# Kernel tuning notes

Measured on AMD Instinct MI355X. Metric: run time of the kernel, lower is better.

The kernel has to match this reference:

```python
import jax, jax.numpy as jnp
import numpy as np

# Production-scale dims
B, DZ, NW, NH, K = 8, 32, 48, 48, 25          # batch, dim_z, grid width/height, n_objects_max
W_RAW = H_RAW = 384.0                          # raw image size
SIZE_MIN, SIZE_MAX = 12.0, 48.0                # object size bounds
SCORE_T, OVER_T = 0.1, 0.3                     # score_threshold, overlap_threshold


def _conv1x1(x, w, b):
    # x: (B, d, nW, nH), w: (o, d), b: (o,) -> (B, o, nW, nH)  [Decoder1by1Linear]
    return jnp.einsum('bdwh,od->bowh', x, w) + b[None, :, None, None]


def _to_box_list(x):
    # (B, nW, nH) -> (N, B) with N = nW*nH, matching convert_to_box_list's permute(2,3,0,1).view
    return jnp.transpose(x, (1, 2, 0)).reshape(-1, x.shape[0])


def _nms(probT, x1, y1, x2, y2, k_max, score_t, over_t):
    # probT, x1..y2: (B, N). Greedy score/overlap NMS -> idx (B, K) int32, mask (B, N) float
    area = (x2 - x1) * (y2 - y1)
    xi1 = jnp.maximum(x1[:, :, None], x1[:, None, :])
    yi1 = jnp.maximum(y1[:, :, None], y1[:, None, :])
    xi2 = jnp.minimum(x2[:, :, None], x2[:, None, :])
    yi2 = jnp.minimum(y2[:, :, None], y2[:, None, :])
    inter = jnp.clip(xi2 - xi1, 0.0) * jnp.clip(yi2 - yi1, 0.0)
    union = area[:, :, None] + area[:, None, :] - inter
    iou = inter / jnp.maximum(union, 1e-8)                      # (B, N, N)
    possible0 = probT > score_t
    Bsz, N = probT.shape
    idx0 = jnp.zeros((Bsz, k_max), jnp.int32)
    val0 = jnp.zeros((Bsz, k_max), bool)

    def body(k, carry):
        possible, idxb, valb = carry
        masked = jnp.where(possible, probT, -jnp.inf)
        sel = jnp.argmax(masked, axis=1).astype(jnp.int32)      # (B,)
        ok = jnp.take_along_axis(possible, sel[:, None], axis=1)[:, 0]
        row = jnp.take_along_axis(iou, sel[:, None, None], axis=1)[:, 0, :]
        possible = possible & (row <= over_t)                   # suppresses sel itself (IoU=1)
        return possible, idxb.at[:, k].set(sel), valb.at[:, k].set(ok)

    _, idxb, valb = jax.lax.fori_loop(0, k_max, body, (possible0, idx0, val0))
    mask = jnp.zeros((Bsz, N), probT.dtype).at[jnp.arange(Bsz)[:, None], idxb].max(
        valb.astype(probT.dtype))
    return idxb, mask


def setup_inputs() -> dict:
    key = jax.random.key(0)
    ks = jax.random.split(key, 5)
    return {
        'zwhere_sample': jax.random.normal(ks[0], (B, DZ, NW, NH), jnp.float32),
        'w_zwhere': 0.2 * jax.random.normal(ks[1], (4, DZ), jnp.float32),
        'b_zwhere': jnp.zeros((4,), jnp.float32),
        'logit_sample': jax.random.normal(ks[2], (B, DZ, NW, NH), jnp.float32),
        'w_logit': 0.2 * jax.random.normal(ks[3], (1, DZ), jnp.float32),
        'b_logit': jnp.zeros((1,), jnp.float32),
        'weight_logits': jax.random.normal(ks[4], (K, B, 1, int(W_RAW), int(H_RAW)), jnp.float32),
    }


def reference(zwhere_sample, w_zwhere, b_zwhere, logit_sample, w_logit, b_logit, weight_logits):
    nW, nH = zwhere_sample.shape[-2:]
    # --- box decoding from zwhere latent map ---
    t = jax.nn.sigmoid(_conv1x1(zwhere_sample, w_zwhere, b_zwhere))  # (B,4,nW,nH)
    tx, ty, tw, th = t[:, 0], t[:, 1], t[:, 2], t[:, 3]
    ix = jnp.arange(nW, dtype=t.dtype)[:, None]   # ij meshgrid rows
    iy = jnp.arange(nH, dtype=t.dtype)[None, :]
    bx = W_RAW * (ix + tx) / nW
    by = H_RAW * (iy + ty) / nH
    bw = SIZE_MIN + (SIZE_MAX - SIZE_MIN) * tw
    bh = SIZE_MIN + (SIZE_MAX - SIZE_MIN) * th
    bx_l, by_l = _to_box_list(bx), _to_box_list(by)   # (N, B)
    bw_l, bh_l = _to_box_list(bw), _to_box_list(bh)
    # --- probability map from logit latent map ---
    p_map = jax.nn.sigmoid(_conv1x1(logit_sample, w_logit, b_logit))  # (B,1,nW,nH)
    prob_all = _to_box_list(p_map[:, 0])              # (N, B)
    probT = prob_all.T                                 # (B, N)
    x1 = (bx_l - 0.5 * bw_l).T
    x2 = (bx_l + 0.5 * bw_l).T
    y1 = (by_l - 0.5 * bh_l).T
    y2 = (by_l + 0.5 * bh_l).T
    # --- NMS under stop_gradient (torch.no_grad in original) ---
    sg = jax.lax.stop_gradient
    idxb, maskB = _nms(sg(probT), sg(x1), sg(y1), sg(x2), sg(y2), K, SCORE_T, OVER_T)
    # prob_few = gather(prob_all * nms_mask, index_top_k): differentiable w.r.t. prob_all
    prob_few = jnp.take_along_axis(probT * maskB, idxb, axis=1).T   # (K, B)
    # --- mask compositing (from_weights_to_masks over the object dim) ---
    big_weight = jax.nn.softplus(weight_logits)       # (K, B, 1, W, H)
    sum_w = jnp.sum(big_weight, axis=0, keepdims=True)
    big_mask = jnp.tanh(sum_w) * (big_weight / jnp.clip(sum_w, 1e-6))
    # probability-weighted masks (downstream compositing)
    return prob_few[:, :, None, None, None] * big_mask  # (K, B, 1, W, H)
```

## Files before the change

kernel.cpp:

```cpp
#include <hip/hip_runtime.h>
#include <math.h>

#define BATCH 8
#define DZ    32
#define NWH   48
#define NBOX  (NWH*NWH)
#define KMAX  25
#define PIX   (384*384)
#define NTOT  (BATCH*NBOX)
#define SLOTS (NBOX/256)

__device__ __forceinline__ float sigm(float x) { return 1.0f / (1.0f + expf(-x)); }

__device__ __forceinline__ float sp_fast(float x) {
    return fmaxf(x, 0.0f) + __logf(1.0f + __expf(-fabsf(x)));
}

__global__ __launch_bounds__(256) void box_kernel(
    const float* __restrict__ z, const float* __restrict__ wz, const float* __restrict__ bz,
    const float* __restrict__ lg, const float* __restrict__ wl, const float* __restrict__ bl,
    float* __restrict__ ws)
{
    int t = blockIdx.x * 256 + threadIdx.x;
    int b = t / 576, j = t % 576;
    int iw = j / 12, ihq = j % 12;

    const float* zb = z  + (((size_t)b * DZ) * NWH + iw) * NWH + ihq * 4;
    const float* lb = lg + (((size_t)b * DZ) * NWH + iw) * NWH + ihq * 4;

    float b0 = bz[0], b1 = bz[1], b2 = bz[2], b3 = bz[3], blg = bl[0];
    float4 a0 = make_float4(b0,b0,b0,b0);
    float4 a1 = make_float4(b1,b1,b1,b1);
    float4 a2 = make_float4(b2,b2,b2,b2);
    float4 a3 = make_float4(b3,b3,b3,b3);
    float4 al = make_float4(blg,blg,blg,blg);

    #pragma unroll 8
    for (int d = 0; d < DZ; ++d) {
        float4 zv = *(const float4*)(zb + (size_t)d * NBOX);
        float4 lv = *(const float4*)(lb + (size_t)d * NBOX);
        float w0 = wz[d], w1 = wz[32+d], w2 = wz[64+d], w3 = wz[96+d], wv = wl[d];
        a0.x += zv.x*w0; a0.y += zv.y*w0; a0.z += zv.z*w0; a0.w += zv.w*w0;
        a1.x += zv.x*w1; a1.y += zv.y*w1; a1.z += zv.z*w1; a1.w += zv.w*w1;
        a2.x += zv.x*w2; a2.y += zv.y*w2; a2.z += zv.z*w2; a2.w += zv.w*w2;
        a3.x += zv.x*w3; a3.y += zv.y*w3; a3.z += zv.z*w3; a3.w += zv.w*w3;
        al.x += lv.x*wv; al.y += lv.y*wv; al.z += lv.z*wv; al.w += lv.w*wv;
    }

    float4 X1, Y1, X2, Y2, P;
    float txv[4] = {a0.x,a0.y,a0.z,a0.w};
    float tyv[4] = {a1.x,a1.y,a1.z,a1.w};
    float twv[4] = {a2.x,a2.y,a2.z,a2.w};
    float thv[4] = {a3.x,a3.y,a3.z,a3.w};
    float alv[4] = {al.x,al.y,al.z,al.w};
    float x1o[4], y1o[4], x2o[4], y2o[4], po[4];
    #pragma unroll
    for (int c = 0; c < 4; ++c) {
        float tx = sigm(txv[c]), ty = sigm(tyv[c]), tw = sigm(twv[c]), th = sigm(thv[c]);
        float bx = 8.0f * ((float)iw + tx);
        float by = 8.0f * ((float)(ihq*4 + c) + ty);
        float bw = 12.0f + 36.0f * tw;
        float bh = 12.0f + 36.0f * th;
        x1o[c] = bx - 0.5f*bw;  y1o[c] = by - 0.5f*bh;
        x2o[c] = bx + 0.5f*bw;  y2o[c] = by + 0.5f*bh;
        po[c]  = sigm(alv[c]);
    }
    X1 = make_float4(x1o[0],x1o[1],x1o[2],x1o[3]);
    Y1 = make_float4(y1o[0],y1o[1],y1o[2],y1o[3]);
    X2 = make_float4(x2o[0],x2o[1],x2o[2],x2o[3]);
    Y2 = make_float4(y2o[0],y2o[1],y2o[2],y2o[3]);
    P  = make_float4(po[0], po[1], po[2], po[3]);

    int o = b * NBOX + iw * NWH + ihq * 4;
    *(float4*)(ws + 0*NTOT + o) = X1;
    *(float4*)(ws + 1*NTOT + o) = Y1;
    *(float4*)(ws + 2*NTOT + o) = X2;
    *(float4*)(ws + 3*NTOT + o) = Y2;
    *(float4*)(ws + 4*NTOT + o) = P;
}

__global__ __launch_bounds__(256) void nms_kernel(const float* __restrict__ ws,
                                                  float* __restrict__ pf)
{
    __shared__ float4 boxS[NBOX];
    __shared__ float  prS[NBOX];
    __shared__ float  redv[4];
    __shared__ int    redi[4];
    __shared__ float4 selB;
    __shared__ int    idxA[KMAX];
    __shared__ int    okA[KMAX];

    int b = blockIdx.x, tid = threadIdx.x;

    float x1r[SLOTS], y1r[SLOTS], x2r[SLOTS], y2r[SLOTS], arr[SLOTS], mkv[SLOTS];
    #pragma unroll
    for (int s = 0; s < SLOTS; ++s) {
        int n = tid + 256*s;
        int o = b * NBOX + n;
        float x1 = ws[0*NTOT+o], y1 = ws[1*NTOT+o], x2 = ws[2*NTOT+o], y2 = ws[3*NTOT+o];
        float p  = ws[4*NTOT+o];
        x1r[s]=x1; y1r[s]=y1; x2r[s]=x2; y2r[s]=y2;
        arr[s] = (x2-x1)*(y2-y1);
        mkv[s] = (p > 0.1f) ? p : -INFINITY;
        boxS[n] = make_float4(x1,y1,x2,y2);
        prS[n]  = p;
    }
    __syncthreads();

    for (int k = 0; k < KMAX; ++k) {
        float4 sb = make_float4(0,0,0,0); float sar = 0.f;
        if (k > 0) { sb = selB; sar = (sb.z - sb.x) * (sb.w - sb.y); }

        float bv = -INFINITY; int bi = 0;
        #pragma unroll
        for (int s = 0; s < SLOTS; ++s) {
            if (k > 0 && mkv[s] != -INFINITY) {
                float xi1 = fmaxf(sb.x, x1r[s]);
                float yi1 = fmaxf(sb.y, y1r[s]);
                float xi2 = fminf(sb.z, x2r[s]);
                float yi2 = fminf(sb.w, y2r[s]);
                float inter = fmaxf(xi2 - xi1, 0.f) * fmaxf(yi2 - yi1, 0.f);
                float uni   = sar + arr[s] - inter;
                float iou   = inter / fmaxf(uni, 1e-8f);
                if (iou > 0.3f) mkv[s] = -INFINITY;
            }
            float v = mkv[s];
            if (v > bv) { bv = v; bi = tid + 256*s; }
        }
        #pragma unroll
        for (int off = 32; off > 0; off >>= 1) {
            float ov = __shfl_down(bv, off);
            int   oi = __shfl_down(bi, off);
            if (ov > bv || (ov == bv && oi < bi)) { bv = ov; bi = oi; }
        }
        if ((tid & 63) == 0) { redv[tid >> 6] = bv; redi[tid >> 6] = bi; }
        __syncthreads();
        if (tid == 0) {
            for (int w = 1; w < 4; ++w)
                if (redv[w] > bv || (redv[w] == bv && redi[w] < bi)) { bv = redv[w]; bi = redi[w]; }
            idxA[k] = bi;
            okA[k]  = (bv != -INFINITY) ? 1 : 0;
            selB    = boxS[bi];
        }
        __syncthreads();
    }

    if (tid == 0) {
        #pragma unroll 1
        for (int k = 0; k < KMAX; ++k) {
            float m = 0.f;
            for (int k2 = 0; k2 < KMAX; ++k2)
                if (idxA[k2] == idxA[k] && okA[k2]) m = 1.f;
            pf[k * BATCH + b] = prS[idxA[k]] * m;
        }
    }
}

__global__ __launch_bounds__(256) void big_kernel(const float* __restrict__ wlg,
                                                  const float* __restrict__ pf,
                                                  float* __restrict__ out)
{
    const size_t stride = (size_t)BATCH * PIX;
    size_t j = ((size_t)blockIdx.x * 256 + threadIdx.x) * 4;
    int b = (int)(j / PIX);

    float4 sp[KMAX];
    float sx = 0.f, sy = 0.f, sz = 0.f, sw = 0.f;
    #pragma unroll
    for (int k = 0; k < KMAX; ++k) {
        float4 v = *(const float4*)(wlg + (size_t)k * stride + j);
        float4 t;
        t.x = sp_fast(v.x); t.y = sp_fast(v.y); t.z = sp_fast(v.z); t.w = sp_fast(v.w);
        sp[k] = t;
        sx += t.x; sy += t.y; sz += t.z; sw += t.w;
    }
    float4 m;
    {
        float tx = __expf(-2.f*sx), ty = __expf(-2.f*sy), tz = __expf(-2.f*sz), tw = __expf(-2.f*sw);
        m.x = (1.f - tx) * __builtin_amdgcn_rcpf(1.f + tx) * __builtin_amdgcn_rcpf(fmaxf(sx, 1e-6f));
        m.y = (1.f - ty) * __builtin_amdgcn_rcpf(1.f + ty) * __builtin_amdgcn_rcpf(fmaxf(sy, 1e-6f));
        m.z = (1.f - tz) * __builtin_amdgcn_rcpf(1.f + tz) * __builtin_amdgcn_rcpf(fmaxf(sz, 1e-6f));
        m.w = (1.f - tw) * __builtin_amdgcn_rcpf(1.f + tw) * __builtin_amdgcn_rcpf(fmaxf(sw, 1e-6f));
    }
    #pragma unroll
    for (int k = 0; k < KMAX; ++k) {
        float c = pf[k * BATCH + b];
        float4 o;
        o.x = c * m.x * sp[k].x;
        o.y = c * m.y * sp[k].y;
        o.z = c * m.z * sp[k].z;
        o.w = c * m.w * sp[k].w;
        *(float4*)(out + (size_t)k * stride + j) = o;
    }
}

extern "C" void kernel_launch(void* const* d_in, const int* in_sizes, int n_in,
                              void* d_out, int out_size, void* d_ws, size_t ws_size,
                              hipStream_t stream)
{
    const float* zwhere = (const float*)d_in[0];
    const float* w_zw   = (const float*)d_in[1];
    const float* b_zw   = (const float*)d_in[2];
    const float* logit  = (const float*)d_in[3];
    const float* w_lg   = (const float*)d_in[4];
    const float* b_lg   = (const float*)d_in[5];
    const float* wlogit = (const float*)d_in[6];
    float* out = (float*)d_out;
    float* ws  = (float*)d_ws;
    float* pf  = ws + 5 * NTOT;

    box_kernel<<<(BATCH*576)/256, 256, 0, stream>>>(zwhere, w_zw, b_zw, logit, w_lg, b_lg, ws);
    nms_kernel<<<BATCH, 256, 0, stream>>>(ws, pf);
    const int n4 = BATCH * PIX / 4;
    big_kernel<<<n4 / 256, 256, 0, stream>>>(wlogit, pf, out);
}
```

Measured before the change: 108.9 us.

## Fuse box and NMS kernels, pack argmax keys, half-precision softplus cache

Measured after the change: 234.9 us. 116% more time.

```diff
diff --git a/kernel.cpp b/kernel.cpp
--- a/kernel.cpp
+++ b/kernel.cpp
@@ -1,4 +1,5 @@
 #include <hip/hip_runtime.h>
+#include <hip/hip_fp16.h>
 #include <math.h>
 
 #define BATCH 8
@@ -7,190 +8,154 @@
 #define NBOX  (NWH*NWH)
 #define KMAX  25
 #define PIX   (384*384)
-#define NTOT  (BATCH*NBOX)
-#define SLOTS (NBOX/256)
+#define NTHR  576
+#define NW9   9
+
+typedef float vfloat4 __attribute__((ext_vector_type(4)));
 
 __device__ __forceinline__ float sigm(float x) { return 1.0f / (1.0f + expf(-x)); }
-
 __device__ __forceinline__ float sp_fast(float x) {
     return fmaxf(x, 0.0f) + __logf(1.0f + __expf(-fabsf(x)));
 }
 
-__global__ __launch_bounds__(256) void box_kernel(
+__global__ __launch_bounds__(NTHR) void boxnms_kernel(
     const float* __restrict__ z, const float* __restrict__ wz, const float* __restrict__ bz,
     const float* __restrict__ lg, const float* __restrict__ wl, const float* __restrict__ bl,
-    float* __restrict__ ws)
+    float* __restrict__ pfT)
 {
-    int t = blockIdx.x * 256 + threadIdx.x;
-    int b = t / 576, j = t % 576;
-    int iw = j / 12, ihq = j % 12;
+    __shared__ vfloat4 boxS[NBOX];
+    __shared__ float   prS[NBOX];
+    __shared__ unsigned long long keyB[2][NW9];
+    __shared__ int idxA[KMAX], okA[KMAX];
+
+    const int b = blockIdx.x, t = threadIdx.x;
+    const int iw = t / 12, ihq = t % 12;
 
     const float* zb = z  + (((size_t)b * DZ) * NWH + iw) * NWH + ihq * 4;
     const float* lb = lg + (((size_t)b * DZ) * NWH + iw) * NWH + ihq * 4;
-
     float b0 = bz[0], b1 = bz[1], b2 = bz[2], b3 = bz[3], blg = bl[0];
-    float4 a0 = make_float4(b0,b0,b0,b0);
-    float4 a1 = make_float4(b1,b1,b1,b1);
-    float4 a2 = make_float4(b2,b2,b2,b2);
-    float4 a3 = make_float4(b3,b3,b3,b3);
-    float4 al = make_float4(blg,blg,blg,blg);
-
+    vfloat4 a0 = {b0,b0,b0,b0}, a1 = {b1,b1,b1,b1}, a2 = {b2,b2,b2,b2},
+            a3 = {b3,b3,b3,b3}, al = {blg,blg,blg,blg};
     #pragma unroll 8
     for (int d = 0; d < DZ; ++d) {
-        float4 zv = *(const float4*)(zb + (size_t)d * NBOX);
-        float4 lv = *(const float4*)(lb + (size_t)d * NBOX);
+        vfloat4 zv = *(const vfloat4*)(zb + (size_t)d * NBOX);
+        vfloat4 lv = *(const vfloat4*)(lb + (size_t)d * NBOX);
         float w0 = wz[d], w1 = wz[32+d], w2 = wz[64+d], w3 = wz[96+d], wv = wl[d];
-        a0.x += zv.x*w0; a0.y += zv.y*w0; a0.z += zv.z*w0; a0.w += zv.w*w0;
-        a1.x += zv.x*w1; a1.y += zv.y*w1; a1.z += zv.z*w1; a1.w += zv.w*w1;
-        a2.x += zv.x*w2; a2.y += zv.y*w2; a2.z += zv.z*w2; a2.w += zv.w*w2;
-        a3.x += zv.x*w3; a3.y += zv.y*w3; a3.z += zv.z*w3; a3.w += zv.w*w3;
-        al.x += lv.x*wv; al.y += lv.y*wv; al.z += lv.z*wv; al.w += lv.w*wv;
+        a0 += zv * w0; a1 += zv * w1; a2 += zv * w2; a3 += zv * w3; al += lv * wv;
     }
 
-    float4 X1, Y1, X2, Y2, P;
-    float txv[4] = {a0.x,a0.y,a0.z,a0.w};
-    float tyv[4] = {a1.x,a1.y,a1.z,a1.w};
-    float twv[4] = {a2.x,a2.y,a2.z,a2.w};
-    float thv[4] = {a3.x,a3.y,a3.z,a3.w};
-    float alv[4] = {al.x,al.y,al.z,al.w};
-    float x1o[4], y1o[4], x2o[4], y2o[4], po[4];
-    #pragma unroll
-    for (int c = 0; c < 4; ++c) {
-        float tx = sigm(txv[c]), ty = sigm(tyv[c]), tw = sigm(twv[c]), th = sigm(thv[c]);
-        float bx = 8.0f * ((float)iw + tx);
-        float by = 8.0f * ((float)(ihq*4 + c) + ty);
-        float bw = 12.0f + 36.0f * tw;
-        float bh = 12.0f + 36.0f * th;
-        x1o[c] = bx - 0.5f*bw;  y1o[c] = by - 0.5f*bh;
-        x2o[c] = bx + 0.5f*bw;  y2o[c] = by + 0.5f*bh;
-        po[c]  = sigm(alv[c]);
+    float x1r[4], y1r[4], x2r[4], y2r[4], arr[4], mkv[4];
+    int   nbs[4];
+    {
+        float t0v[4] = {a0.x,a0.y,a0.z,a0.w};
+        float t1v[4] = {a1.x,a1.y,a1.z,a1.w};
+        float t2v[4] = {a2.x,a2.y,a2.z,a2.w};
+        float t3v[4] = {a3.x,a3.y,a3.z,a3.w};
+        float alv[4] = {al.x,al.y,al.z,al.w};
+        #pragma unroll
+        for (int c = 0; c < 4; ++c) {
+            float tx = sigm(t0v[c]), ty = sigm(t1v[c]), tw = sigm(t2v[c]), th = sigm(t3v[c]);
+            float bx = 8.0f * ((float)iw + tx);
+            float by = 8.0f * ((float)(ihq*4 + c) + ty);
+            float bw = 12.0f + 36.0f * tw;
+            float bh = 12.0f + 36.0f * th;
+            float x1 = bx - 0.5f*bw, y1 = by - 0.5f*bh, x2 = bx + 0.5f*bw, y2 = by + 0.5f*bh;
+            float p  = sigm(alv[c]);
+            int   n  = iw * NWH + ihq*4 + c;
+            x1r[c]=x1; y1r[c]=y1; x2r[c]=x2; y2r[c]=y2;
+            arr[c] = (x2-x1)*(y2-y1);
+            mkv[c] = (p > 0.1f) ? p : -INFINITY;
+            nbs[c] = n;
+            boxS[n] = (vfloat4){x1,y1,x2,y2};
+            prS[n]  = p;
+        }
     }
-    X1 = make_float4(x1o[0],x1o[1],x1o[2],x1o[3]);
-    Y1 = make_float4(y1o[0],y1o[1],y1o[2],y1o[3]);
-    X2 = make_float4(x2o[0],x2o[1],x2o[2],x2o[3]);
-    Y2 = make_float4(y2o[0],y2o[1],y2o[2],y2o[3]);
-    P  = make_float4(po[0], po[1], po[2], po[3]);
 
-    int o = b * NBOX + iw * NWH + ihq * 4;
-    *(float4*)(ws + 0*NTOT + o) = X1;
-    *(float4*)(ws + 1*NTOT + o) = Y1;
-    *(float4*)(ws + 2*NTOT + o) = X2;
-    *(float4*)(ws + 3*NTOT + o) = Y2;
-    *(float4*)(ws + 4*NTOT + o) = P;
-}
-
-__global__ __launch_bounds__(256) void nms_kernel(const float* __restrict__ ws,
-                                                  float* __restrict__ pf)
-{
-    __shared__ float4 boxS[NBOX];
-    __shared__ float  prS[NBOX];
-    __shared__ float  redv[4];
-    __shared__ int    redi[4];
-    __shared__ float4 selB;
-    __shared__ int    idxA[KMAX];
-    __shared__ int    okA[KMAX];
-
-    int b = blockIdx.x, tid = threadIdx.x;
-
-    float x1r[SLOTS], y1r[SLOTS], x2r[SLOTS], y2r[SLOTS], arr[SLOTS], mkv[SLOTS];
-    #pragma unroll
-    for (int s = 0; s < SLOTS; ++s) {
-        int n = tid + 256*s;
-        int o = b * NBOX + n;
-        float x1 = ws[0*NTOT+o], y1 = ws[1*NTOT+o], x2 = ws[2*NTOT+o], y2 = ws[3*NTOT+o];
-        float p  = ws[4*NTOT+o];
-        x1r[s]=x1; y1r[s]=y1; x2r[s]=x2; y2r[s]=y2;
-        arr[s] = (x2-x1)*(y2-y1);
-        mkv[s] = (p > 0.1f) ? p : -INFINITY;
-        boxS[n] = make_float4(x1,y1,x2,y2);
-        prS[n]  = p;
-    }
-    __syncthreads();
-
+    float sx1=0.f, sy1=0.f, sx2=0.f, sy2=0.f, sar=0.f;
     for (int k = 0; k < KMAX; ++k) {
-        float4 sb = make_float4(0,0,0,0); float sar = 0.f;
-        if (k > 0) { sb = selB; sar = (sb.z - sb.x) * (sb.w - sb.y); }
-
-        float bv = -INFINITY; int bi = 0;
+        unsigned long long best = 0ULL;
         #pragma unroll
-        for (int s = 0; s < SLOTS; ++s) {
-            if (k > 0 && mkv[s] != -INFINITY) {
-                float xi1 = fmaxf(sb.x, x1r[s]);
-                float yi1 = fmaxf(sb.y, y1r[s]);
-                float xi2 = fminf(sb.z, x2r[s]);
-                float yi2 = fminf(sb.w, y2r[s]);
+        for (int c = 0; c < 4; ++c) {
+            if (k > 0 && mkv[c] != -INFINITY) {
+                float xi1 = fmaxf(sx1, x1r[c]);
+                float yi1 = fmaxf(sy1, y1r[c]);
+                float xi2 = fminf(sx2, x2r[c]);
+                float yi2 = fminf(sy2, y2r[c]);
                 float inter = fmaxf(xi2 - xi1, 0.f) * fmaxf(yi2 - yi1, 0.f);
-                float uni   = sar + arr[s] - inter;
+                float uni   = sar + arr[c] - inter;
                 float iou   = inter / fmaxf(uni, 1e-8f);
-                if (iou > 0.3f) mkv[s] = -INFINITY;
+                if (iou > 0.3f) mkv[c] = -INFINITY;
             }
-            float v = mkv[s];
-            if (v > bv) { bv = v; bi = tid + 256*s; }
+            if (mkv[c] != -INFINITY) {
+                unsigned long long kk =
+                    ((unsigned long long)__float_as_uint(mkv[c]) << 32) | (unsigned int)(~nbs[c]);
+                if (kk > best) best = kk;
+            }
         }
         #pragma unroll
         for (int off = 32; off > 0; off >>= 1) {
-            float ov = __shfl_down(bv, off);
-            int   oi = __shfl_down(bi, off);
-            if (ov > bv || (ov == bv && oi < bi)) { bv = ov; bi = oi; }
+            unsigned long long o = __shfl_down(best, off);
+            if (o > best) best = o;
         }
-        if ((tid & 63) == 0) { redv[tid >> 6] = bv; redi[tid >> 6] = bi; }
+        if ((t & 63) == 0) keyB[k & 1][t >> 6] = best;
         __syncthreads();
-        if (tid == 0) {
-            for (int w = 1; w < 4; ++w)
-                if (redv[w] > bv || (redv[w] == bv && redi[w] < bi)) { bv = redv[w]; bi = redi[w]; }
-            idxA[k] = bi;
-            okA[k]  = (bv != -INFINITY) ? 1 : 0;
-            selB    = boxS[bi];
+        unsigned long long m = keyB[k & 1][0];
+        #pragma unroll
+        for (int w = 1; w < NW9; ++w) {
+            unsigned long long o = keyB[k & 1][w];
+            if (o > m) m = o;
         }
-        __syncthreads();
+        int sel = (m == 0ULL) ? 0 : (int)(~(unsigned int)(m & 0xFFFFFFFFULL));
+        if (t == 0) { idxA[k] = sel; okA[k] = (m != 0ULL); }
+        vfloat4 sb = boxS[sel];
+        sx1 = sb.x; sy1 = sb.y; sx2 = sb.z; sy2 = sb.w;
+        sar = (sx2 - sx1) * (sy2 - sy1);
     }
 
-    if (tid == 0) {
+    if (t == 0) {
         #pragma unroll 1
         for (int k = 0; k < KMAX; ++k) {
-            float m = 0.f;
+            float mm = 0.f;
             for (int k2 = 0; k2 < KMAX; ++k2)
-                if (idxA[k2] == idxA[k] && okA[k2]) m = 1.f;
-            pf[k * BATCH + b] = prS[idxA[k]] * m;
+                if (idxA[k2] == idxA[k] && okA[k2]) mm = 1.f;
+            pfT[b * 32 + k] = prS[idxA[k]] * mm;
         }
     }
 }
 
-__global__ __launch_bounds__(256) void big_kernel(const float* __restrict__ wlg,
-                                                  const float* __restrict__ pf,
-                                                  float* __restrict__ out)
+__global__ __launch_bounds__(256, 6) void big_kernel(const float* __restrict__ wlg,
+                                                     const float* __restrict__ pfT,
+                                                     float* __restrict__ out)
 {
     const size_t stride = (size_t)BATCH * PIX;
     size_t j = ((size_t)blockIdx.x * 256 + threadIdx.x) * 4;
     int b = (int)(j / PIX);
 
-    float4 sp[KMAX];
+    __half2 sp01[KMAX], sp23[KMAX];
     float sx = 0.f, sy = 0.f, sz = 0.f, sw = 0.f;
     #pragma unroll
     for (int k = 0; k < KMAX; ++k) {
-        float4 v = *(const float4*)(wlg + (size_t)k * stride + j);
-        float4 t;
-        t.x = sp_fast(v.x); t.y = sp_fast(v.y); t.z = sp_fast(v.z); t.w = sp_fast(v.w);
-        sp[k] = t;
-        sx += t.x; sy += t.y; sz += t.z; sw += t.w;
+        vfloat4 v = *(const vfloat4*)(wlg + (size_t)k * stride + j);
+        float tx = sp_fast(v.x), ty = sp_fast(v.y), tz = sp_fast(v.z), tw = sp_fast(v.w);
+        sx += tx; sy += ty; sz += tz; sw += tw;
+        sp01[k] = __floats2half2_rn(tx, ty);
+        sp23[k] = __floats2half2_rn(tz, tw);
     }
-    float4 m;
+    float mx, my, mz, mw;
     {
-        float tx = __expf(-2.f*sx), ty = __expf(-2.f*sy), tz = __expf(-2.f*sz), tw = __expf(-2.f*sw);
-        m.x = (1.f - tx) * __builtin_amdgcn_rcpf(1.f + tx) * __builtin_amdgcn_rcpf(fmaxf(sx, 1e-6f));
-        m.y = (1.f - ty) * __builtin_amdgcn_rcpf(1.f + ty) * __builtin_amdgcn_rcpf(fmaxf(sy, 1e-6f));
-        m.z = (1.f - tz) * __builtin_amdgcn_rcpf(1.f + tz) * __builtin_amdgcn_rcpf(fmaxf(sz, 1e-6f));
-        m.w = (1.f - tw) * __builtin_amdgcn_rcpf(1.f + tw) * __builtin_amdgcn_rcpf(fmaxf(sw, 1e-6f));
+        float ex = __expf(-2.f*sx), ey = __expf(-2.f*sy), ez = __expf(-2.f*sz), ew = __expf(-2.f*sw);
+        mx = (1.f - ex) * __builtin_amdgcn_rcpf(1.f + ex) * __builtin_amdgcn_rcpf(fmaxf(sx, 1e-6f));
+        my = (1.f - ey) * __builtin_amdgcn_rcpf(1.f + ey) * __builtin_amdgcn_rcpf(fmaxf(sy, 1e-6f));
+        mz = (1.f - ez) * __builtin_amdgcn_rcpf(1.f + ez) * __builtin_amdgcn_rcpf(fmaxf(sz, 1e-6f));
+        mw = (1.f - ew) * __builtin_amdgcn_rcpf(1.f + ew) * __builtin_amdgcn_rcpf(fmaxf(sw, 1e-6f));
     }
     #pragma unroll
     for (int k = 0; k < KMAX; ++k) {
-        float c = pf[k * BATCH + b];
-        float4 o;
-        o.x = c * m.x * sp[k].x;
-        o.y = c * m.y * sp[k].y;
-        o.z = c * m.z * sp[k].z;
-        o.w = c * m.w * sp[k].w;
-        *(float4*)(out + (size_t)k * stride + j) = o;
+        float c = pfT[b * 32 + k];
+        float2 a = __half22float2(sp01[k]);
+        float2 d = __half22float2(sp23[k]);
+        vfloat4 o = { c * mx * a.x, c * my * a.y, c * mz * d.x, c * mw * d.y };
+        __builtin_nontemporal_store(o, (vfloat4*)(out + (size_t)k * stride + j));
     }
 }
 
@@ -206,11 +171,9 @@
     const float* b_lg   = (const float*)d_in[5];
     const float* wlogit = (const float*)d_in[6];
     float* out = (float*)d_out;
-    float* ws  = (float*)d_ws;
-    float* pf  = ws + 5 * NTOT;
+    float* pfT = (float*)d_ws;
 
-    box_kernel<<<(BATCH*576)/256, 256, 0, stream>>>(zwhere, w_zw, b_zw, logit, w_lg, b_lg, ws);
-    nms_kernel<<<BATCH, 256, 0, stream>>>(ws, pf);
+    boxnms_kernel<<<BATCH, NTHR, 0, stream>>>(zwhere, w_zw, b_zw, logit, w_lg, b_lg, pfT);
     const int n4 = BATCH * PIX / 4;
-    big_kernel<<<n4 / 256, 256, 0, stream>>>(wlogit, pf, out);
+    big_kernel<<<n4 / 256, 256, 0, stream>>>(wlogit, pfT, out);
 }
```
